# Kernel optimization log

Hardware: AMD Instinct MI355X
Metric: run time of the kernel (lower is better)

Reference implementation:

```python
import jax, jax.numpy as jnp
import numpy as np

N = 4096      # nodes
F = 128       # input feature dim
HEADS = 8     # attention_num
U = 8         # units per head


def setup_inputs() -> dict:
    key = jax.random.key(0)
    k_a, k_h, k_w, k_al, k_ar = jax.random.split(key, 5)
    A = jax.random.randint(k_a, (N, N), 0, 2).astype(jnp.float32)   # dense 0/1 adjacency
    H = jax.random.normal(k_h, (N, F), dtype=jnp.float32)
    W = jax.random.normal(k_w, (HEADS, F, U), dtype=jnp.float32) * 0.1
    a_left = jax.random.normal(k_al, (HEADS, U), dtype=jnp.float32) * 0.1
    a_right = jax.random.normal(k_ar, (HEADS, U), dtype=jnp.float32) * 0.1
    return {"A": A, "H": H, "W": W, "a_left": a_left, "a_right": a_right}


def reference(A, H, W, a_left, a_right):
    # Per-head attention logits: E[h,i,j] = e_left[h,i] + e_right[h,j]
    e_l = jnp.einsum('nf,hfu,hu->hn', H, W, a_left)    # [HEADS, N]
    e_r = jnp.einsum('nf,hfu,hu->hn', H, W, a_right)   # [HEADS, N]
    E = e_l[:, :, None] + e_r[:, None, :]              # [HEADS, N, N]
    # Faithful to original: denominator uses exp(E * A) (zeros in A -> exp(0)=1)
    denom = jnp.sum(jnp.exp(E * A[None]), axis=-1, keepdims=True)   # [HEADS, N, 1]
    Alpha = jnp.exp(E) / denom * A[None]               # masked attention weights
    # Aggregate then project: elu(Alpha @ H @ W) per head
    out = jax.nn.elu(jnp.einsum('hij,jf,hfu->hiu', Alpha, H, W))    # [HEADS, N, U]
    # is_output_layer=False -> concat heads along feature dim: [N, HEADS*U]
    return jnp.transpose(out, (1, 0, 2)).reshape(H.shape[0], HEADS * U)
```

## Files before the change

### kernel.cpp

```cpp
#include <hip/hip_runtime.h>
#include <hip/hip_bf16.h>

#define NN 4096
#define FF 128
#define HEADS 8
#define UU 8
#define NC 80

typedef __attribute__((ext_vector_type(4))) float float4v;
typedef __attribute__((ext_vector_type(4))) unsigned int uint4v;
typedef __attribute__((ext_vector_type(8))) short short8;

__global__ __launch_bounds__(64) void gat_prep(const float* __restrict__ H,
                                               const float* __restrict__ W,
                                               const float* __restrict__ al,
                                               const float* __restrict__ ar,
                                               float* __restrict__ expEl,
                                               __hip_bfloat16* __restrict__ Bp)
{
    const int j = blockIdx.x;
    const int t = threadIdx.x;
    const int h = t >> 3, u = t & 7;

    __shared__ float hrow[FF];
    for (int f = t; f < FF; f += 64) hrow[f] = H[j * FF + f];
    __syncthreads();

    float acc = 0.f;
    const float* Wp = W + (size_t)h * FF * UU + u;
    #pragma unroll 4
    for (int f = 0; f < FF; ++f) acc += hrow[f] * Wp[(size_t)f * UU];

    float vr = acc * ar[h * UU + u];
    float vl = acc * al[h * UU + u];
    #pragma unroll
    for (int s = 1; s < 8; s <<= 1) { vr += __shfl_xor(vr, s); vl += __shfl_xor(vl, s); }
    const float er = expf(vr);
    const float el = expf(vl);
    if (u == 0) expEl[h * NN + j] = el;

    const float er_b = __shfl(er, (t & 7) * 8);

    const int kt = j >> 5, q = (j >> 3) & 3, j8 = j & 7;
    const size_t base = ((size_t)(kt * 4 + q) * NC) * 8 + j8;
    Bp[base + (size_t)(h * 8 + u) * 8] = __float2bfloat16(er * acc);

    if (t < 16) {
        const int c = 64 + t;
        float v;
        if (t < 8)       v = er_b;
        else if (t == 8) v = 1.0f;
        else             v = 0.0f;
        Bp[base + (size_t)c * 8] = __float2bfloat16(v);
    }
}

__global__ __launch_bounds__(256) void gat_gemm(const float* __restrict__ A,
                                                const __hip_bfloat16* __restrict__ Bp,
                                                float* __restrict__ Cp,
                                                int ktiles)
{
    const int rb   = blockIdx.x;
    const int kc   = blockIdx.y;
    const int wave = threadIdx.x >> 6;
    const int lane = threadIdx.x & 63;
    const int m16  = lane & 15;
    const int q    = lane >> 4;
    const int row0 = rb * 64 + wave * 16;

    float4v acc[5] = {};

    const int k0 = kc * (ktiles * 32);
    const unsigned int* Au = (const unsigned int*)A;
    const short* Bs = (const short*)Bp;

    for (int kt = 0; kt < ktiles; ++kt) {
        const int kk = k0 + kt * 32;
        const unsigned int* arow = Au + (size_t)(row0 + m16) * NN + kk + q * 8;
        uint4v a0 = *(const uint4v*)arow;
        uint4v a1 = *(const uint4v*)(arow + 4);
        short8 afrag;
        afrag[0] = (short)(a0[0] >> 16); afrag[1] = (short)(a0[1] >> 16);
        afrag[2] = (short)(a0[2] >> 16); afrag[3] = (short)(a0[3] >> 16);
        afrag[4] = (short)(a1[0] >> 16); afrag[5] = (short)(a1[1] >> 16);
        afrag[6] = (short)(a1[2] >> 16); afrag[7] = (short)(a1[3] >> 16);

        const int ktg = kk >> 5;
        const short8* bbase = (const short8*)(Bs + ((size_t)(ktg * 4 + q) * NC) * 8);
        #pragma unroll
        for (int nt = 0; nt < 5; ++nt) {
            short8 bfrag = bbase[nt * 16 + m16];
            acc[nt] = __builtin_amdgcn_mfma_f32_16x16x32_bf16(afrag, bfrag, acc[nt], 0, 0, 0);
        }
    }

    float* cbase = Cp + (size_t)kc * NN * NC;
    #pragma unroll
    for (int nt = 0; nt < 5; ++nt) {
        #pragma unroll
        for (int r = 0; r < 4; ++r) {
            const int row = row0 + q * 4 + r;
            const int col = nt * 16 + m16;
            cbase[(size_t)row * NC + col] = acc[nt][r];
        }
    }
}

__global__ __launch_bounds__(256) void gat_epilogue(const float* __restrict__ Cp,
                                                    const float* __restrict__ expEl,
                                                    float* __restrict__ out,
                                                    int KC)
{
    const int idx = blockIdx.x * 256 + threadIdx.x;
    const int i = idx >> 6;
    const int c = idx & 63;
    const int h = c >> 3;

    float T = 0.f, S = 0.f, dg = 0.f;
    for (int kc = 0; kc < KC; ++kc) {
        const float* row = Cp + ((size_t)kc * NN + i) * NC;
        T  += row[c];
        S  += row[64 + h];
        dg += row[72];
    }
    const float el = expEl[h * NN + i];
    const float denom = ((float)NN - dg) + el * S;
    const float x = el * T / denom;
    const float y = x > 0.f ? x : expf(x) - 1.f;
    out[idx] = y;
}

extern "C" void kernel_launch(void* const* d_in, const int* in_sizes, int n_in,
                              void* d_out, int out_size, void* d_ws, size_t ws_size,
                              hipStream_t stream) {
    const float* A  = (const float*)d_in[0];
    const float* H  = (const float*)d_in[1];
    const float* W  = (const float*)d_in[2];
    const float* al = (const float*)d_in[3];
    const float* ar = (const float*)d_in[4];
    float* out = (float*)d_out;

    float* expEl = (float*)d_ws;
    __hip_bfloat16* Bp = (__hip_bfloat16*)((char*)d_ws + 131072);
    float* Cp = (float*)((char*)d_ws + 131072 + 655360);

    const size_t fixed = 131072 + 655360;
    int KC = 8;
    while (KC > 1 && fixed + (size_t)KC * NN * NC * 4 > ws_size) KC >>= 1;
    const int ktiles = NN / (KC * 32);

    gat_prep<<<NN, 64, 0, stream>>>(H, W, al, ar, expEl, Bp);
    gat_gemm<<<dim3(NN / 64, KC), 256, 0, stream>>>(A, Bp, Cp, ktiles);
    gat_epilogue<<<NN * 64 / 256, 256, 0, stream>>>(Cp, expEl, out, KC);
}
```

Baseline: 125.3 us.

## Batch prep over 16 nodes with shared W, prefetch A tiles, raise K-split

The prep kernel now handles 16 nodes per 256-thread block and stages W and H rows in shared memory, so W is loaded once per block rather than re-read from global memory per node. The GEMM loop software-prefetches the next A tile into registers while the current MFMAs run, to hide global load latency. The K-split count rises from 8 to 16 to launch more GEMM blocks and fill more CUs, at the cost of a larger partial-sum buffer and more reduction work in the epilogue.

```diff
diff --git a/kernel.cpp b/kernel.cpp
--- a/kernel.cpp
+++ b/kernel.cpp
@@ -3,55 +3,65 @@
 
 #define NN 4096
 #define FF 128
-#define HEADS 8
-#define UU 8
 #define NC 80
 
 typedef __attribute__((ext_vector_type(4))) float float4v;
 typedef __attribute__((ext_vector_type(4))) unsigned int uint4v;
 typedef __attribute__((ext_vector_type(8))) short short8;
 
-__global__ __launch_bounds__(64) void gat_prep(const float* __restrict__ H,
-                                               const float* __restrict__ W,
-                                               const float* __restrict__ al,
-                                               const float* __restrict__ ar,
-                                               float* __restrict__ expEl,
-                                               __hip_bfloat16* __restrict__ Bp)
+__global__ __launch_bounds__(256) void gat_prep(const float* __restrict__ H,
+                                                const float* __restrict__ W,
+                                                const float* __restrict__ al,
+                                                const float* __restrict__ ar,
+                                                float* __restrict__ expEl,
+                                                __hip_bfloat16* __restrict__ Bp)
 {
-    const int j = blockIdx.x;
-    const int t = threadIdx.x;
-    const int h = t >> 3, u = t & 7;
+    __shared__ float Ws[FF * 64];
+    __shared__ float Hs[16 * FF];
+    const int t  = threadIdx.x;
+    const int j0 = blockIdx.x * 16;
 
-    __shared__ float hrow[FF];
-    for (int f = t; f < FF; f += 64) hrow[f] = H[j * FF + f];
+    #pragma unroll
+    for (int i = 0; i < 32; ++i) {
+        const int q = t + i * 256;
+        const int f = q >> 6, hu = q & 63;
+        Ws[q] = W[(size_t)(hu >> 3) * (FF * 8) + f * 8 + (hu & 7)];
+    }
+    #pragma unroll
+    for (int i = 0; i < 8; ++i) {
+        const int q = t + i * 256;
+        Hs[q] = H[(size_t)j0 * FF + q];
+    }
     __syncthreads();
 
-    float acc = 0.f;
-    const float* Wp = W + (size_t)h * FF * UU + u;
-    #pragma unroll 4
-    for (int f = 0; f < FF; ++f) acc += hrow[f] * Wp[(size_t)f * UU];
+    const int wave = t >> 6, lane = t & 63;
+    const int h = lane >> 3, u = lane & 7;
+    const float a_r = ar[lane], a_l = al[lane];
 
-    float vr = acc * ar[h * UU + u];
-    float vl = acc * al[h * UU + u];
     #pragma unroll
-    for (int s = 1; s < 8; s <<= 1) { vr += __shfl_xor(vr, s); vl += __shfl_xor(vl, s); }
-    const float er = expf(vr);
-    const float el = expf(vl);
-    if (u == 0) expEl[h * NN + j] = el;
+    for (int jj = 0; jj < 4; ++jj) {
+        const int jl = wave * 4 + jj;
+        const int j  = j0 + jl;
+        float acc = 0.f;
+        #pragma unroll 8
+        for (int f = 0; f < FF; ++f)
+            acc += Hs[jl * FF + f] * Ws[f * 64 + lane];
 
-    const float er_b = __shfl(er, (t & 7) * 8);
+        float vr = acc * a_r, vl = acc * a_l;
+        #pragma unroll
+        for (int s = 1; s < 8; s <<= 1) { vr += __shfl_xor(vr, s); vl += __shfl_xor(vl, s); }
+        const float er = expf(vr);
+        const float el = expf(vl);
+        if (u == 0) expEl[h * NN + j] = el;
+        const float er_b = __shfl(er, u * 8);
 
-    const int kt = j >> 5, q = (j >> 3) & 3, j8 = j & 7;
-    const size_t base = ((size_t)(kt * 4 + q) * NC) * 8 + j8;
-    Bp[base + (size_t)(h * 8 + u) * 8] = __float2bfloat16(er * acc);
-
-    if (t < 16) {
-        const int c = 64 + t;
-        float v;
-        if (t < 8)       v = er_b;
-        else if (t == 8) v = 1.0f;
-        else             v = 0.0f;
-        Bp[base + (size_t)c * 8] = __float2bfloat16(v);
+        const int kt = j >> 5, q = (j >> 3) & 3, j8 = j & 7;
+        const size_t base = ((size_t)(kt * 4 + q) * NC) * 8 + j8;
+        Bp[base + (size_t)lane * 8] = __float2bfloat16(er * acc);
+        if (lane < 16) {
+            const float v = (lane < 8) ? er_b : (lane == 8 ? 1.0f : 0.0f);
+            Bp[base + (size_t)(64 + lane) * 8] = __float2bfloat16(v);
+        }
     }
 }
 
@@ -73,17 +83,23 @@
     const int k0 = kc * (ktiles * 32);
     const unsigned int* Au = (const unsigned int*)A;
     const short* Bs = (const short*)Bp;
+    const unsigned int* arow = Au + (size_t)(row0 + m16) * NN + q * 8;
+
+    uint4v a0 = *(const uint4v*)(arow + k0);
+    uint4v a1 = *(const uint4v*)(arow + k0 + 4);
 
     for (int kt = 0; kt < ktiles; ++kt) {
         const int kk = k0 + kt * 32;
-        const unsigned int* arow = Au + (size_t)(row0 + m16) * NN + kk + q * 8;
-        uint4v a0 = *(const uint4v*)arow;
-        uint4v a1 = *(const uint4v*)(arow + 4);
         short8 afrag;
         afrag[0] = (short)(a0[0] >> 16); afrag[1] = (short)(a0[1] >> 16);
         afrag[2] = (short)(a0[2] >> 16); afrag[3] = (short)(a0[3] >> 16);
         afrag[4] = (short)(a1[0] >> 16); afrag[5] = (short)(a1[1] >> 16);
         afrag[6] = (short)(a1[2] >> 16); afrag[7] = (short)(a1[3] >> 16);
+
+        if (kt + 1 < ktiles) {
+            a0 = *(const uint4v*)(arow + kk + 32);
+            a1 = *(const uint4v*)(arow + kk + 36);
+        }
 
         const int ktg = kk >> 5;
         const short8* bbase = (const short8*)(Bs + ((size_t)(ktg * 4 + q) * NC) * 8);
@@ -145,11 +161,11 @@
     float* Cp = (float*)((char*)d_ws + 131072 + 655360);
 
     const size_t fixed = 131072 + 655360;
-    int KC = 8;
+    int KC = 16;
     while (KC > 1 && fixed + (size_t)KC * NN * NC * 4 > ws_size) KC >>= 1;
     const int ktiles = NN / (KC * 32);
 
-    gat_prep<<<NN, 64, 0, stream>>>(H, W, al, ar, expEl, Bp);
+    gat_prep<<<NN / 16, 256, 0, stream>>>(H, W, al, ar, expEl, Bp);
     gat_gemm<<<dim3(NN / 64, KC), 256, 0, stream>>>(A, Bp, Cp, ktiles);
     gat_epilogue<<<NN * 64 / 256, 256, 0, stream>>>(Cp, expEl, out, KC);
 }
```

Result: no change. 125.4 us (+0.1%).
